# Kernel optimization log

Hardware: AMD Instinct MI355X
Metric: run time of the kernel (lower is better)

Reference implementation:

```python
import jax, jax.numpy as jnp
import numpy as np

B, P1, P2 = 16, 25, 24          # batch, patch-grid rows (+cls row), cols
E0, E1, E2 = 8, 8, 16           # 3-way factorized embed dim (total 1024)
H1, H2, H3 = 2, 2, 4            # 3-way head split (16 heads)
X, Y, Z = E0 // H1, E1 // H2, E2 // H3   # per-head factor dims (4,4,4)
SCALE = float((X * Y * Z) ** -0.5)        # head_dim = 64


def _tcl(x, w0, w1, w2, b):
    # Tensor Contraction Layer: mode-wise linear maps on the 3 embed modes.
    return jnp.einsum('bpqxyz,ax,cy,dz->bpqacd', x, w0, w1, w2) + b


def setup_inputs() -> dict:
    key = jax.random.key(0)
    ks = jax.random.split(key, 17)
    inp = {"x": jax.random.normal(ks[0], (B, P1, P2, E0, E1, E2), jnp.float32)}
    i = 1
    for nm in ("q", "k", "v", "o"):
        inp[f"{nm}_w0"] = jax.random.normal(ks[i], (E0, E0), jnp.float32) * (E0 ** -0.5); i += 1
        inp[f"{nm}_w1"] = jax.random.normal(ks[i], (E1, E1), jnp.float32) * (E1 ** -0.5); i += 1
        inp[f"{nm}_w2"] = jax.random.normal(ks[i], (E2, E2), jnp.float32) * (E2 ** -0.5); i += 1
        inp[f"{nm}_b"] = jax.random.normal(ks[i], (E0, E1, E2), jnp.float32) * 0.02; i += 1
    return inp


def _split_heads(t):
    t = t.reshape(B, P1, P2, X, H1, Y, H2, Z, H3)
    return t.transpose(0, 1, 2, 4, 6, 8, 3, 5, 7)


def reference(x,
              q_w0, q_w1, q_w2, q_b,
              k_w0, k_w1, k_w2, k_b,
              v_w0, v_w1, v_w2, v_b,
              o_w0, o_w1, o_w2, o_b):
    q = _tcl(x, q_w0, q_w1, q_w2, q_b)
    k = _tcl(x, k_w0, k_w1, k_w2, k_b)
    v = _tcl(x, v_w0, v_w1, v_w2, v_b)
    Q, K, V = _split_heads(q), _split_heads(k), _split_heads(v)
    # scores over all (p1,p2) x (m,n) token pairs, per (h1,h2,h3) head
    attn = jnp.einsum('bpqdefxyz,bmndefxyz->bdefpqmn', Q, K) * SCALE
    a = attn.reshape(B, H1, H2, H3, P1, P2, P1 * P2)
    a = jax.nn.softmax(a, axis=-1).reshape(attn.shape)
    out = jnp.einsum('bdefpqmn,bmndefxyz->bdefpqxyz', a, V)
    # b h1 h2 h3 p q x y z -> b p q (x h1)(y h2)(z h3)
    out = out.transpose(0, 4, 5, 6, 1, 7, 2, 8, 3).reshape(B, P1, P2, E0, E1, E2)
    return _tcl(out, o_w0, o_w1, o_w2, o_b)
```

## Files before the change

kernel.cpp:

```cpp
#include <hip/hip_runtime.h>

#define S   600
#define NB  16
#define NH  16
#define HD  64
#define QSCALE 0.18033688011112042f

#define LDT 20

typedef _Float16 f16x8 __attribute__((ext_vector_type(8)));
typedef float f32x4 __attribute__((ext_vector_type(4)));

__global__ __launch_bounds__(256) void tcl_qkv_kernel(
    const float* __restrict__ x,
    const float* __restrict__ qw0, const float* __restrict__ qw1,
    const float* __restrict__ qw2, const float* __restrict__ qb,
    const float* __restrict__ kw0, const float* __restrict__ kw1,
    const float* __restrict__ kw2, const float* __restrict__ kb,
    const float* __restrict__ vw0, const float* __restrict__ vw1,
    const float* __restrict__ vw2, const float* __restrict__ vb,
    _Float16* __restrict__ Qh, _Float16* __restrict__ Kh,
    _Float16* __restrict__ Vh)
{
  __shared__ __align__(16) float t1s[4][64 * LDT];
  __shared__ __align__(16) float t2s[4][64 * LDT];

  const int tid = threadIdx.x;
  const int wv = tid >> 6, lane = tid & 63;
  const int tok = blockIdx.x * 4 + wv;
  const int b = tok / S, t = tok - b * S;
  const int q = lane >> 3, zp = lane & 7;
  float* __restrict__ t1 = t1s[wv];
  float* __restrict__ t2 = t2s[wv];

  float2 xc[8];
  #pragma unroll
  for (int xx = 0; xx < 8; ++xx)
    xc[xx] = *(const float2*)&x[(size_t)tok * 1024 + xx * 128 + q * 16 + zp * 2];

  const int xs = lane >> 4;
  const int h1 = (lane >> 3) & 1;
  const int cc = lane & 7;
  const int ys = cc >> 1, h2 = cc & 1;

  const float* W0[3] = {qw0, kw0, vw0};
  const float* W1[3] = {qw1, kw1, vw1};
  const float* W2[3] = {qw2, kw2, vw2};
  const float* BB[3] = {qb, kb, vb};
  _Float16* OUT[3] = {Qh, Kh, Vh};

  #pragma unroll
  for (int p = 0; p < 3; ++p) {
    const float* __restrict__ w0 = W0[p];
    const float* __restrict__ w1 = W1[p];
    const float* __restrict__ w2 = W2[p];
    const float* __restrict__ bb = BB[p];
    _Float16* __restrict__ op = OUT[p];

    #pragma unroll
    for (int a = 0; a < 8; ++a) {
      float2 r = make_float2(0.f, 0.f);
      #pragma unroll
      for (int xx = 0; xx < 8; ++xx) {
        const float w = w0[a * 8 + xx];
        r.x = fmaf(w, xc[xx].x, r.x);
        r.y = fmaf(w, xc[xx].y, r.y);
      }
      *(float2*)&t1[(a * 8 + q) * LDT + zp * 2] = r;
    }
    __builtin_amdgcn_wave_barrier();

    float2 t1r[8];
    #pragma unroll
    for (int y = 0; y < 8; ++y)
      t1r[y] = *(float2*)&t1[(q * 8 + y) * LDT + zp * 2];
    #pragma unroll
    for (int c = 0; c < 8; ++c) {
      float2 r = make_float2(0.f, 0.f);
      #pragma unroll
      for (int y = 0; y < 8; ++y) {
        const float w = w1[c * 8 + y];
        r.x = fmaf(w, t1r[y].x, r.x);
        r.y = fmaf(w, t1r[y].y, r.y);
      }
      *(float2*)&t2[(q * 8 + c) * LDT + zp * 2] = r;
    }
    __builtin_amdgcn_wave_barrier();

    float t2r[16];
    #pragma unroll
    for (int k = 0; k < 4; ++k)
      *(float4*)&t2r[k * 4] = *(float4*)&t2[lane * LDT + k * 4];
    float bias[16];
    #pragma unroll
    for (int k = 0; k < 4; ++k)
      *(float4*)&bias[k * 4] = *(const float4*)&bb[lane * 16 + k * 4];
    float o[16];
    #pragma unroll
    for (int d = 0; d < 16; ++d) {
      float acc = 0.f;
      #pragma unroll
      for (int j = 0; j < 16; ++j)
        acc = fmaf(w2[d * 16 + j], t2r[j], acc);
      o[d] = acc + bias[d];
    }
    const float sc = (p == 0) ? QSCALE : 1.0f;
    #pragma unroll
    for (int h3 = 0; h3 < 4; ++h3) {
      union { _Float16 hh[4]; uint2 u; } pk;
      #pragma unroll
      for (int z = 0; z < 4; ++z)
        pk.hh[z] = (_Float16)(o[4 * z + h3] * sc);
      const int head = h1 * 8 + h2 * 4 + h3;
      *(uint2*)&op[((size_t)((b * NH + head) * S + t)) * HD + xs * 16 + ys * 4]
          = pk.u;
    }
    __builtin_amdgcn_wave_barrier();
  }
}

__global__ __launch_bounds__(256) void vtrans_kernel(
    const _Float16* __restrict__ Vh, _Float16* __restrict__ Vt)
{
  __shared__ __align__(16) _Float16 tile[64 * 64];
  const int tid = threadIdx.x;
  const int tt = blockIdx.x, h = blockIdx.y, b = blockIdx.z;
  const size_t rbase = (size_t)(b * NH + h) * S * HD;
  const size_t wbase = (size_t)(b * NH + h) * HD * S;
  const int t0 = tt * 64;

  #pragma unroll
  for (int hp = 0; hp < 2; ++hp) {
    const int u = hp * 256 + tid;
    const int r = u >> 3, ch = u & 7;
    f16x8 v = {0, 0, 0, 0, 0, 0, 0, 0};
    if (t0 + r < S) v = *(const f16x8*)&Vh[rbase + (size_t)(t0 + r) * HD + ch * 8];
    *(f16x8*)&tile[r * 64 + ((ch ^ ((r ^ (r >> 3)) & 7)) * 8)] = v;
  }
  __syncthreads();
  #pragma unroll
  for (int hp = 0; hp < 2; ++hp) {
    const int w = hp * 256 + tid;
    const int d = w >> 3, tc = w & 7;
    if (t0 + tc * 8 + 8 <= S) {
      const int cd = d >> 3;
      union { _Float16 hh[8]; f16x8 v; } g;
      #pragma unroll
      for (int e = 0; e < 8; ++e) {
        const int r = tc * 8 + e;
        g.hh[e] = tile[r * 64 + ((cd ^ ((r ^ (r >> 3)) & 7)) * 8) + (d & 7)];
      }
      *(f16x8*)&Vt[wbase + (size_t)d * S + t0 + tc * 8] = g.v;
    }
  }
}

__device__ __forceinline__ void gload16(const _Float16* g, _Float16* l) {
  __builtin_amdgcn_global_load_lds(
      (const __attribute__((address_space(1))) unsigned int*)g,
      (__attribute__((address_space(3))) unsigned int*)l, 16, 0, 0);
}

template<bool TAIL>
__device__ __forceinline__ void attn_step(
    const _Float16* __restrict__ Ks, const _Float16* __restrict__ Vs,
    _Float16* __restrict__ Pw,
    const f16x8 qf0, const f16x8 qf1,
    f32x4 (&po)[4], float& mrow, float& lrow,
    const int lr, const int lg)
{
  constexpr int NMT = TAIL ? 2 : 4;
  f32x4 accs[NMT];
  #pragma unroll
  for (int mt = 0; mt < NMT; ++mt) accs[mt] = (f32x4){0.f, 0.f, 0.f, 0.f};
  __builtin_amdgcn_s_setprio(1);
  #pragma unroll
  for (int c = 0; c < 2; ++c) {
    const f16x8 qf = c ? qf1 : qf0;
    #pragma unroll
    for (int mt = 0; mt < NMT; ++mt) {
      const int krow = mt * 16 + lr;
      const f16x8 kf = *(const f16x8*)
          &Ks[krow * 64 + (((4 * c + lg) ^ (krow & 7)) * 8)];
      accs[mt] = __builtin_amdgcn_mfma_f32_16x16x32_f16(kf, qf, accs[mt], 0, 0, 0);
    }
  }
  __builtin_amdgcn_s_setprio(0);
  float sv[NMT][4];
  #pragma unroll
  for (int mt = 0; mt < NMT; ++mt)
    #pragma unroll
    for (int r = 0; r < 4; ++r) {
      float s = accs[mt][r];
      if (TAIL && mt == 1) s = (lg < 2) ? s : -1e30f;
      sv[mt][r] = s;
    }
  float tmax;
  {
    const float a = fmaxf(fmaxf(sv[0][0], sv[0][1]), fmaxf(sv[0][2], sv[0][3]));
    const float b = fmaxf(fmaxf(sv[1][0], sv[1][1]), fmaxf(sv[1][2], sv[1][3]));
    if (TAIL) {
      tmax = fmaxf(a, b);
    } else {
      const float c2 = fmaxf(fmaxf(sv[2][0], sv[2][1]), fmaxf(sv[2][2], sv[2][3]));
      const float d2 = fmaxf(fmaxf(sv[3][0], sv[3][1]), fmaxf(sv[3][2], sv[3][3]));
      tmax = fmaxf(fmaxf(a, b), fmaxf(c2, d2));
    }
  }
  tmax = fmaxf(tmax, __shfl_xor(tmax, 16));
  tmax = fmaxf(tmax, __shfl_xor(tmax, 32));
  if (!__all(tmax - mrow <= 11.0f)) {
    const float mn = fmaxf(mrow, tmax);
    const float corr = __builtin_amdgcn_exp2f(mrow - mn);
    lrow *= corr;
    #pragma unroll
    for (int dt = 0; dt < 4; ++dt) {
      po[dt][0] *= corr; po[dt][1] *= corr;
      po[dt][2] *= corr; po[dt][3] *= corr;
    }
    mrow = mn;
  }
  _Float16 ph[NMT][4];
  float rsv[NMT];
  #pragma unroll
  for (int mt = 0; mt < NMT; ++mt) {
    const float e0 = __builtin_amdgcn_exp2f(sv[mt][0] - mrow);
    const float e1 = __builtin_amdgcn_exp2f(sv[mt][1] - mrow);
    const float e2 = __builtin_amdgcn_exp2f(sv[mt][2] - mrow);
    const float e3 = __builtin_amdgcn_exp2f(sv[mt][3] - mrow);
    ph[mt][0] = (_Float16)e0; ph[mt][1] = (_Float16)e1;
    ph[mt][2] = (_Float16)e2; ph[mt][3] = (_Float16)e3;
    rsv[mt] = (e0 + e1) + (e2 + e3);
  }
  float rs = TAIL ? (rsv[0] + rsv[1]) : ((rsv[0] + rsv[1]) + (rsv[2] + rsv[3]));
  rs += __shfl_xor(rs, 16);
  rs += __shfl_xor(rs, 32);
  lrow += rs;
  #pragma unroll
  for (int mt = 0; mt < NMT; ++mt) {
    union { _Float16 hh[4]; unsigned long long u; } pk;
    pk.hh[0] = ph[mt][0]; pk.hh[1] = ph[mt][1];
    pk.hh[2] = ph[mt][2]; pk.hh[3] = ph[mt][3];
    const int idx = lr * 64 + (((2 * mt + (lg >> 1)) ^ (lr & 7)) * 8)
                  + (lg & 1) * 4;
    *(unsigned long long*)&Pw[idx] = pk.u;
  }
  __builtin_amdgcn_wave_barrier();
  __builtin_amdgcn_s_setprio(1);
  #pragma unroll
  for (int c = 0; c < (TAIL ? 1 : 2); ++c) {
    const f16x8 pf = *(const f16x8*)&Pw[lr * 64 + (((4 * c + lg) ^ (lr & 7)) * 8)];
    #pragma unroll
    for (int dt = 0; dt < 4; ++dt) {
      const int drow = dt * 16 + lr;
      const f16x8 vf = *(const f16x8*)
          &Vs[drow * 64 + (((4 * c + lg) ^ (drow & 7)) * 8)];
      po[dt] = __builtin_amdgcn_mfma_f32_16x16x32_f16(vf, pf, po[dt], 0, 0, 0);
    }
  }
  __builtin_amdgcn_s_setprio(0);
}

__global__ __launch_bounds__(256, 4) void attn_mfma_kernel(
    const _Float16* __restrict__ Qh, const _Float16* __restrict__ Kh,
    const _Float16* __restrict__ Vt, float* __restrict__ Og)
{
  __shared__ __align__(16) union {
    struct {
      _Float16 K[2][64 * 64];
      _Float16 V[2][64 * 64];
      _Float16 P[4][16 * 64];
    } m;
    float ot[4][64 * 17];
  } sm;

  const int tid = threadIdx.x;
  const int lane = tid & 63;
  const int wv = tid >> 6;
  const int id = blockIdx.x;
  const int idx = id >> 3;
  const int bh = (id & 7) * 32 + idx / 10;
  const int qt = idx - (idx / 10) * 10;
  const size_t base  = (size_t)bh * S * HD;
  const size_t vbase = (size_t)bh * HD * S;
  const int lr = lane & 15;
  const int lg = lane >> 4;

  const int qrow_l = qt * 64 + wv * 16 + lr;
  const int qrow = (qrow_l < S) ? qrow_l : (S - 1);
  const f16x8 qf0 = *(const f16x8*)&Qh[base + (size_t)qrow * HD + lg * 8];
  const f16x8 qf1 = *(const f16x8*)&Qh[base + (size_t)qrow * HD + 32 + lg * 8];

  f32x4 po[4] = {{0.f,0.f,0.f,0.f},{0.f,0.f,0.f,0.f},
                 {0.f,0.f,0.f,0.f},{0.f,0.f,0.f,0.f}};
  float mrow = -1e30f, lrow = 0.f;

  const int sr = lane >> 3, ss = lane & 7;
  const int swz8 = (ss ^ sr) * 8;
  const int c0 = wv, c1 = wv + 4;
  const _Float16* kg0 = Kh + base + (size_t)(c0 * 8 + sr) * HD + swz8;
  const _Float16* kg1 = Kh + base + (size_t)(c1 * 8 + sr) * HD + swz8;
  const _Float16* vg0 = Vt + vbase + (size_t)(c0 * 8 + sr) * S + swz8;
  const _Float16* vg1 = Vt + vbase + (size_t)(c1 * 8 + sr) * S + swz8;

  auto gload_tile = [&](int kt, int b) {
    const int kb = kt * 64;
    gload16(kg0 + (size_t)kb * HD, &sm.m.K[b][c0 * 512]);
    gload16(kg1 + (size_t)kb * HD, &sm.m.K[b][c1 * 512]);
    gload16(vg0 + kb, &sm.m.V[b][c0 * 512]);
    gload16(vg1 + kb, &sm.m.V[b][c1 * 512]);
  };

  gload_tile(0, 0);
  #pragma unroll 2
  for (int kt = 0; kt < 9; ++kt) {
    const int b = kt & 1;
    __syncthreads();
    gload_tile(kt + 1, b ^ 1);
    attn_step<false>(&sm.m.K[b][0], &sm.m.V[b][0], &sm.m.P[wv][0],
                     qf0, qf1, po, mrow, lrow, lr, lg);
  }
  __syncthreads();
  for (int u = tid; u < 320; u += 256) {
    const int row = u / 5, kc = 3 + u % 5;
    *(f16x8*)&sm.m.V[1][row * 64 + ((kc ^ (row & 7)) * 8)] =
        (f16x8){0, 0, 0, 0, 0, 0, 0, 0};
  }
  __syncthreads();
  attn_step<true>(&sm.m.K[1][0], &sm.m.V[1][0], &sm.m.P[wv][0],
                  qf0, qf1, po, mrow, lrow, lr, lg);
  __syncthreads();

  const float invl = 1.0f / lrow;
  #pragma unroll
  for (int dt = 0; dt < 4; ++dt)
    #pragma unroll
    for (int r = 0; r < 4; ++r)
      sm.ot[wv][(dt * 16 + 4 * lg + r) * 17 + lr] = po[dt][r] * invl;
  __builtin_amdgcn_wave_barrier();
  #pragma unroll
  for (int ps = 0; ps < 4; ++ps) {
    const int qr = ps * 4 + lg;
    const int gq = qt * 64 + wv * 16 + qr;
    if (gq < S) {
      const int d0 = lr * 4;
      float4 o4;
      o4.x = sm.ot[wv][(d0 + 0) * 17 + qr];
      o4.y = sm.ot[wv][(d0 + 1) * 17 + qr];
      o4.z = sm.ot[wv][(d0 + 2) * 17 + qr];
      o4.w = sm.ot[wv][(d0 + 3) * 17 + qr];
      *(float4*)&Og[base + (size_t)gq * HD + d0] = o4;
    }
  }
}

__global__ __launch_bounds__(256) void tcl_out_kernel(
    const float* __restrict__ Og,
    const float* __restrict__ ow0, const float* __restrict__ ow1,
    const float* __restrict__ ow2, const float* __restrict__ ob,
    float* __restrict__ out)
{
  __shared__ __align__(16) float t1s[4][64 * LDT];
  __shared__ __align__(16) float t2s[4][64 * LDT];

  const int tid = threadIdx.x;
  const int wv = tid >> 6, lane = tid & 63;
  const int tok = blockIdx.x * 4 + wv;
  const int b = tok / S, t = tok - b * S;
  const int q = lane >> 3, zp = lane & 7;
  float* __restrict__ t1 = t1s[wv];
  float* __restrict__ t2 = t2s[wv];

  float2 xc[8];
  {
    const int h2g = q & 1, yg = q >> 1;
    const int h3g = 2 * (zp & 1), zg = zp >> 1;
    #pragma unroll
    for (int xx = 0; xx < 8; ++xx) {
      const int headb = (xx & 1) * 8 + h2g * 4 + h3g;
      const size_t off = ((size_t)((b * NH + headb) * S + t)) * HD
                       + (xx >> 1) * 16 + yg * 4 + zg;
      xc[xx].x = Og[off];
      xc[xx].y = Og[off + (size_t)S * HD];
    }
  }

  #pragma unroll
  for (int a = 0; a < 8; ++a) {
    float2 r = make_float2(0.f, 0.f);
    #pragma unroll
    for (int xx = 0; xx < 8; ++xx) {
      const float w = ow0[a * 8 + xx];
      r.x = fmaf(w, xc[xx].x, r.x);
      r.y = fmaf(w, xc[xx].y, r.y);
    }
    *(float2*)&t1[(a * 8 + q) * LDT + zp * 2] = r;
  }
  __builtin_amdgcn_wave_barrier();

  float2 t1r[8];
  #pragma unroll
  for (int y = 0; y < 8; ++y)
    t1r[y] = *(float2*)&t1[(q * 8 + y) * LDT + zp * 2];
  #pragma unroll
  for (int c = 0; c < 8; ++c) {
    float2 r = make_float2(0.f, 0.f);
    #pragma unroll
    for (int y = 0; y < 8; ++y) {
      const float w = ow1[c * 8 + y];
      r.x = fmaf(w, t1r[y].x, r.x);
      r.y = fmaf(w, t1r[y].y, r.y);
    }
    *(float2*)&t2[(q * 8 + c) * LDT + zp * 2] = r;
  }
  __builtin_amdgcn_wave_barrier();

  float t2r[16];
  #pragma unroll
  for (int k = 0; k < 4; ++k)
    *(float4*)&t2r[k * 4] = *(float4*)&t2[lane * LDT + k * 4];
  float bias[16];
  #pragma unroll
  for (int k = 0; k < 4; ++k)
    *(float4*)&bias[k * 4] = *(const float4*)&ob[lane * 16 + k * 4];
  float o[16];
  #pragma unroll
  for (int d = 0; d < 16; ++d) {
    float acc = 0.f;
    #pragma unroll
    for (int j = 0; j < 16; ++j)
      acc = fmaf(ow2[d * 16 + j], t2r[j], acc);
    o[d] = acc + bias[d];
  }
  #pragma unroll
  for (int k = 0; k < 4; ++k) {
    const float4 res = make_float4(o[4 * k], o[4 * k + 1],
                                   o[4 * k + 2], o[4 * k + 3]);
    *(float4*)&out[(size_t)tok * 1024 + lane * 16 + k * 4] = res;
  }
}

extern "C" void kernel_launch(void* const* d_in, const int* in_sizes, int n_in,
                              void* d_out, int out_size, void* d_ws, size_t ws_size,
                              hipStream_t stream) {
  const float* x   = (const float*)d_in[0];
  const float* qw0 = (const float*)d_in[1];
  const float* qw1 = (const float*)d_in[2];
  const float* qw2 = (const float*)d_in[3];
  const float* qb  = (const float*)d_in[4];
  const float* kw0 = (const float*)d_in[5];
  const float* kw1 = (const float*)d_in[6];
  const float* kw2 = (const float*)d_in[7];
  const float* kb  = (const float*)d_in[8];
  const float* vw0 = (const float*)d_in[9];
  const float* vw1 = (const float*)d_in[10];
  const float* vw2 = (const float*)d_in[11];
  const float* vb  = (const float*)d_in[12];
  const float* ow0 = (const float*)d_in[13];
  const float* ow1 = (const float*)d_in[14];
  const float* ow2 = (const float*)d_in[15];
  const float* ob  = (const float*)d_in[16];

  const size_t N = (size_t)NB * NH * S * HD;
  _Float16* Qh  = (_Float16*)d_ws;
  _Float16* Kh  = Qh + N;
  _Float16* Vth = Kh + N;
  _Float16* Vh  = Vth + N;
  float*    O   = (float*)Vh;

  tcl_qkv_kernel<<<dim3(NB * S / 4), 256, 0, stream>>>(
      x, qw0, qw1, qw2, qb, kw0, kw1, kw2, kb, vw0, vw1, vw2, vb, Qh, Kh, Vh);
  vtrans_kernel<<<dim3(10, NH, NB), 256, 0, stream>>>(Vh, Vth);
  attn_mfma_kernel<<<dim3(2560), 256, 0, stream>>>(Qh, Kh, Vth, O);
  tcl_out_kernel<<<dim3(NB * S / 4), 256, 0, stream>>>(O, ow0, ow1, ow2, ob,
                                                       (float*)d_out);
}
```

Before: 119.1 us.

## Switch attention to 32x32x16 MFMA with 32 query rows per wave

Rewrites the attention inner step to use 32x32x16 f16 MFMA instead of 16x16x32, giving each wave 32 query rows and each block 128, which halves the grid to 1280 blocks. Each K/V tile read from LDS now serves twice as many query rows, and the per-row softmax shuffles drop to a single xor. The P buffer, output staging layout and tail masking are reworked to match. In exchange, per-thread register use rises (two 16-float score accumulators plus two 16-float outputs), which may reduce occupancy, and the coarser 128-row tiling wastes more work on the final 600-row tile.

```diff
diff --git a/kernel.cpp b/kernel.cpp
--- a/kernel.cpp
+++ b/kernel.cpp
@@ -10,6 +10,7 @@
 
 typedef _Float16 f16x8 __attribute__((ext_vector_type(8)));
 typedef float f32x4 __attribute__((ext_vector_type(4)));
+typedef float f32x16 __attribute__((ext_vector_type(16)));
 
 __global__ __launch_bounds__(256) void tcl_qkv_kernel(
     const float* __restrict__ x,
@@ -161,104 +162,116 @@
       (__attribute__((address_space(3))) unsigned int*)l, 16, 0, 0);
 }
 
+#define ZERO16 {0.f,0.f,0.f,0.f,0.f,0.f,0.f,0.f,0.f,0.f,0.f,0.f,0.f,0.f,0.f,0.f}
+
 template<bool TAIL>
-__device__ __forceinline__ void attn_step(
+__device__ __forceinline__ void attn_step32(
     const _Float16* __restrict__ Ks, const _Float16* __restrict__ Vs,
     _Float16* __restrict__ Pw,
-    const f16x8 qf0, const f16x8 qf1,
-    f32x4 (&po)[4], float& mrow, float& lrow,
-    const int lr, const int lg)
+    const f16x8 (&qf)[4],
+    f32x16 (&po)[2], float& mrow, float& lrow,
+    const int lq, const int lh)
 {
-  constexpr int NMT = TAIL ? 2 : 4;
-  f32x4 accs[NMT];
-  #pragma unroll
-  for (int mt = 0; mt < NMT; ++mt) accs[mt] = (f32x4){0.f, 0.f, 0.f, 0.f};
+  const int ksw = lq & 7;
+  f32x16 a0 = ZERO16, a1 = ZERO16;
   __builtin_amdgcn_s_setprio(1);
   #pragma unroll
-  for (int c = 0; c < 2; ++c) {
-    const f16x8 qf = c ? qf1 : qf0;
-    #pragma unroll
-    for (int mt = 0; mt < NMT; ++mt) {
-      const int krow = mt * 16 + lr;
-      const f16x8 kf = *(const f16x8*)
-          &Ks[krow * 64 + (((4 * c + lg) ^ (krow & 7)) * 8)];
-      accs[mt] = __builtin_amdgcn_mfma_f32_16x16x32_f16(kf, qf, accs[mt], 0, 0, 0);
+  for (int kc = 0; kc < 4; ++kc) {
+    const int slot = ((kc * 2 + lh) ^ ksw) * 8;
+    const f16x8 k0 = *(const f16x8*)&Ks[lq * 64 + slot];
+    a0 = __builtin_amdgcn_mfma_f32_32x32x16_f16(k0, qf[kc], a0, 0, 0, 0);
+    if (!TAIL) {
+      const f16x8 k1 = *(const f16x8*)&Ks[(32 + lq) * 64 + slot];
+      a1 = __builtin_amdgcn_mfma_f32_32x32x16_f16(k1, qf[kc], a1, 0, 0, 0);
     }
   }
   __builtin_amdgcn_s_setprio(0);
-  float sv[NMT][4];
-  #pragma unroll
-  for (int mt = 0; mt < NMT; ++mt)
-    #pragma unroll
-    for (int r = 0; r < 4; ++r) {
-      float s = accs[mt][r];
-      if (TAIL && mt == 1) s = (lg < 2) ? s : -1e30f;
-      sv[mt][r] = s;
-    }
-  float tmax;
-  {
-    const float a = fmaxf(fmaxf(sv[0][0], sv[0][1]), fmaxf(sv[0][2], sv[0][3]));
-    const float b = fmaxf(fmaxf(sv[1][0], sv[1][1]), fmaxf(sv[1][2], sv[1][3]));
-    if (TAIL) {
-      tmax = fmaxf(a, b);
-    } else {
-      const float c2 = fmaxf(fmaxf(sv[2][0], sv[2][1]), fmaxf(sv[2][2], sv[2][3]));
-      const float d2 = fmaxf(fmaxf(sv[3][0], sv[3][1]), fmaxf(sv[3][2], sv[3][3]));
-      tmax = fmaxf(fmaxf(a, b), fmaxf(c2, d2));
-    }
-  }
-  tmax = fmaxf(tmax, __shfl_xor(tmax, 16));
+  float sv0[16], sv1[16];
+  float tmax = -1e30f;
+  #pragma unroll
+  for (int r = 0; r < 16; ++r) {
+    float s = a0[r];
+    if (TAIL && r >= 12) s = -1e30f;
+    sv0[r] = s;
+    tmax = fmaxf(tmax, s);
+  }
+  if (!TAIL) {
+    #pragma unroll
+    for (int r = 0; r < 16; ++r) { sv1[r] = a1[r]; tmax = fmaxf(tmax, sv1[r]); }
+  }
   tmax = fmaxf(tmax, __shfl_xor(tmax, 32));
   if (!__all(tmax - mrow <= 11.0f)) {
     const float mn = fmaxf(mrow, tmax);
     const float corr = __builtin_amdgcn_exp2f(mrow - mn);
     lrow *= corr;
-    #pragma unroll
-    for (int dt = 0; dt < 4; ++dt) {
-      po[dt][0] *= corr; po[dt][1] *= corr;
-      po[dt][2] *= corr; po[dt][3] *= corr;
-    }
+    po[0] *= corr;
+    po[1] *= corr;
     mrow = mn;
   }
-  _Float16 ph[NMT][4];
-  float rsv[NMT];
-  #pragma unroll
-  for (int mt = 0; mt < NMT; ++mt) {
-    const float e0 = __builtin_amdgcn_exp2f(sv[mt][0] - mrow);
-    const float e1 = __builtin_amdgcn_exp2f(sv[mt][1] - mrow);
-    const float e2 = __builtin_amdgcn_exp2f(sv[mt][2] - mrow);
-    const float e3 = __builtin_amdgcn_exp2f(sv[mt][3] - mrow);
-    ph[mt][0] = (_Float16)e0; ph[mt][1] = (_Float16)e1;
-    ph[mt][2] = (_Float16)e2; ph[mt][3] = (_Float16)e3;
-    rsv[mt] = (e0 + e1) + (e2 + e3);
-  }
-  float rs = TAIL ? (rsv[0] + rsv[1]) : ((rsv[0] + rsv[1]) + (rsv[2] + rsv[3]));
-  rs += __shfl_xor(rs, 16);
+  float rs = 0.f;
+  {
+    _Float16 ph[16];
+    #pragma unroll
+    for (int r = 0; r < 16; ++r) {
+      const float e = __builtin_amdgcn_exp2f(sv0[r] - mrow);
+      rs += e;
+      ph[r] = (_Float16)e;
+    }
+    #pragma unroll
+    for (int g = 0; g < 4; ++g) {
+      union { _Float16 hh[4]; unsigned long long u; } pk;
+      pk.hh[0] = ph[4*g]; pk.hh[1] = ph[4*g+1];
+      pk.hh[2] = ph[4*g+2]; pk.hh[3] = ph[4*g+3];
+      *(unsigned long long*)&Pw[lq * 32 + ((g ^ (lq & 3)) * 8) + lh * 4] = pk.u;
+    }
+    __builtin_amdgcn_wave_barrier();
+    __builtin_amdgcn_s_setprio(1);
+    #pragma unroll
+    for (int kc2 = 0; kc2 < 2; ++kc2) {
+      const f16x8 pf = *(const f16x8*)
+          &Pw[lq * 32 + (((kc2 * 2 + lh) ^ (lq & 3)) * 8)];
+      #pragma unroll
+      for (int db = 0; db < 2; ++db) {
+        const f16x8 vf = *(const f16x8*)
+            &Vs[(db * 32 + lq) * 64 + (((kc2 * 2 + lh) ^ ksw) * 8)];
+        po[db] = __builtin_amdgcn_mfma_f32_32x32x16_f16(vf, pf, po[db], 0, 0, 0);
+      }
+    }
+    __builtin_amdgcn_s_setprio(0);
+  }
+  if (!TAIL) {
+    __builtin_amdgcn_wave_barrier();
+    _Float16 ph[16];
+    #pragma unroll
+    for (int r = 0; r < 16; ++r) {
+      const float e = __builtin_amdgcn_exp2f(sv1[r] - mrow);
+      rs += e;
+      ph[r] = (_Float16)e;
+    }
+    #pragma unroll
+    for (int g = 0; g < 4; ++g) {
+      union { _Float16 hh[4]; unsigned long long u; } pk;
+      pk.hh[0] = ph[4*g]; pk.hh[1] = ph[4*g+1];
+      pk.hh[2] = ph[4*g+2]; pk.hh[3] = ph[4*g+3];
+      *(unsigned long long*)&Pw[lq * 32 + ((g ^ (lq & 3)) * 8) + lh * 4] = pk.u;
+    }
+    __builtin_amdgcn_wave_barrier();
+    __builtin_amdgcn_s_setprio(1);
+    #pragma unroll
+    for (int kc2 = 0; kc2 < 2; ++kc2) {
+      const f16x8 pf = *(const f16x8*)
+          &Pw[lq * 32 + (((kc2 * 2 + lh) ^ (lq & 3)) * 8)];
+      #pragma unroll
+      for (int db = 0; db < 2; ++db) {
+        const f16x8 vf = *(const f16x8*)
+            &Vs[(db * 32 + lq) * 64 + (((4 + kc2 * 2 + lh) ^ ksw) * 8)];
+        po[db] = __builtin_amdgcn_mfma_f32_32x32x16_f16(vf, pf, po[db], 0, 0, 0);
+      }
+    }
+    __builtin_amdgcn_s_setprio(0);
+  }
   rs += __shfl_xor(rs, 32);
   lrow += rs;
-  #pragma unroll
-  for (int mt = 0; mt < NMT; ++mt) {
-    union { _Float16 hh[4]; unsigned long long u; } pk;
-    pk.hh[0] = ph[mt][0]; pk.hh[1] = ph[mt][1];
-    pk.hh[2] = ph[mt][2]; pk.hh[3] = ph[mt][3];
-    const int idx = lr * 64 + (((2 * mt + (lg >> 1)) ^ (lr & 7)) * 8)
-                  + (lg & 1) * 4;
-    *(unsigned long long*)&Pw[idx] = pk.u;
-  }
-  __builtin_amdgcn_wave_barrier();
-  __builtin_amdgcn_s_setprio(1);
-  #pragma unroll
-  for (int c = 0; c < (TAIL ? 1 : 2); ++c) {
-    const f16x8 pf = *(const f16x8*)&Pw[lr * 64 + (((4 * c + lg) ^ (lr & 7)) * 8)];
-    #pragma unroll
-    for (int dt = 0; dt < 4; ++dt) {
-      const int drow = dt * 16 + lr;
-      const f16x8 vf = *(const f16x8*)
-          &Vs[drow * 64 + (((4 * c + lg) ^ (drow & 7)) * 8)];
-      po[dt] = __builtin_amdgcn_mfma_f32_16x16x32_f16(vf, pf, po[dt], 0, 0, 0);
-    }
-  }
-  __builtin_amdgcn_s_setprio(0);
 }
 
 __global__ __launch_bounds__(256, 4) void attn_mfma_kernel(
@@ -269,9 +282,9 @@
     struct {
       _Float16 K[2][64 * 64];
       _Float16 V[2][64 * 64];
-      _Float16 P[4][16 * 64];
+      _Float16 P[4][32 * 32];
     } m;
-    float ot[4][64 * 17];
+    float ot[4][32 * 68];
   } sm;
 
   const int tid = threadIdx.x;
@@ -279,20 +292,21 @@
   const int wv = tid >> 6;
   const int id = blockIdx.x;
   const int idx = id >> 3;
-  const int bh = (id & 7) * 32 + idx / 10;
-  const int qt = idx - (idx / 10) * 10;
+  const int bh = (id & 7) * 32 + idx / 5;
+  const int qt = idx - (idx / 5) * 5;
   const size_t base  = (size_t)bh * S * HD;
   const size_t vbase = (size_t)bh * HD * S;
-  const int lr = lane & 15;
-  const int lg = lane >> 4;
-
-  const int qrow_l = qt * 64 + wv * 16 + lr;
+  const int lq = lane & 31;
+  const int lh = lane >> 5;
+
+  const int qrow_l = qt * 128 + wv * 32 + lq;
   const int qrow = (qrow_l < S) ? qrow_l : (S - 1);
-  const f16x8 qf0 = *(const f16x8*)&Qh[base + (size_t)qrow * HD + lg * 8];
-  const f16x8 qf1 = *(const f16x8*)&Qh[base + (size_t)qrow * HD + 32 + lg * 8];
-
-  f32x4 po[4] = {{0.f,0.f,0.f,0.f},{0.f,0.f,0.f,0.f},
-                 {0.f,0.f,0.f,0.f},{0.f,0.f,0.f,0.f}};
+  f16x8 qf[4];
+  #pragma unroll
+  for (int kc = 0; kc < 4; ++kc)
+    qf[kc] = *(const f16x8*)&Qh[base + (size_t)qrow * HD + kc * 16 + lh * 8];
+
+  f32x16 po[2] = {ZERO16, ZERO16};
   float mrow = -1e30f, lrow = 0.f;
 
   const int sr = lane >> 3, ss = lane & 7;
@@ -317,39 +331,43 @@
     const int b = kt & 1;
     __syncthreads();
     gload_tile(kt + 1, b ^ 1);
-    attn_step<false>(&sm.m.K[b][0], &sm.m.V[b][0], &sm.m.P[wv][0],
-                     qf0, qf1, po, mrow, lrow, lr, lg);
+    attn_step32<false>(&sm.m.K[b][0], &sm.m.V[b][0], &sm.m.P[wv][0],
+                       qf, po, mrow, lrow, lq, lh);
   }
   __syncthreads();
   for (int u = tid; u < 320; u += 256) {
-    const int row = u / 5, kc = 3 + u % 5;
-    *(f16x8*)&sm.m.V[1][row * 64 + ((kc ^ (row & 7)) * 8)] =
+    const int row = u / 5, ch = 3 + u % 5;
+    *(f16x8*)&sm.m.V[1][row * 64 + ((ch ^ (row & 7)) * 8)] =
         (f16x8){0, 0, 0, 0, 0, 0, 0, 0};
   }
   __syncthreads();
-  attn_step<true>(&sm.m.K[1][0], &sm.m.V[1][0], &sm.m.P[wv][0],
-                  qf0, qf1, po, mrow, lrow, lr, lg);
+  attn_step32<true>(&sm.m.K[1][0], &sm.m.V[1][0], &sm.m.P[wv][0],
+                    qf, po, mrow, lrow, lq, lh);
   __syncthreads();
 
   const float invl = 1.0f / lrow;
-  #pragma unroll
-  for (int dt = 0; dt < 4; ++dt)
-    #pragma unroll
-    for (int r = 0; r < 4; ++r)
-      sm.ot[wv][(dt * 16 + 4 * lg + r) * 17 + lr] = po[dt][r] * invl;
+  float* otw = &sm.ot[wv][0];
+  #pragma unroll
+  for (int db = 0; db < 2; ++db)
+    #pragma unroll
+    for (int g = 0; g < 4; ++g) {
+      float4 v;
+      v.x = po[db][4*g]   * invl;
+      v.y = po[db][4*g+1] * invl;
+      v.z = po[db][4*g+2] * invl;
+      v.w = po[db][4*g+3] * invl;
+      *(float4*)&otw[lq * 68 + db * 32 + g * 8 + lh * 4] = v;
+    }
   __builtin_amdgcn_wave_barrier();
-  #pragma unroll
-  for (int ps = 0; ps < 4; ++ps) {
-    const int qr = ps * 4 + lg;
-    const int gq = qt * 64 + wv * 16 + qr;
+  {
+    const int r = lane >> 1, half = lane & 1;
+    const int gq = qt * 128 + wv * 32 + r;
     if (gq < S) {
-      const int d0 = lr * 4;
-      float4 o4;
-      o4.x = sm.ot[wv][(d0 + 0) * 17 + qr];
-      o4.y = sm.ot[wv][(d0 + 1) * 17 + qr];
-      o4.z = sm.ot[wv][(d0 + 2) * 17 + qr];
-      o4.w = sm.ot[wv][(d0 + 3) * 17 + qr];
-      *(float4*)&Og[base + (size_t)gq * HD + d0] = o4;
+      #pragma unroll
+      for (int k2 = 0; k2 < 8; ++k2) {
+        const float4 v = *(float4*)&otw[r * 68 + half * 32 + k2 * 4];
+        *(float4*)&Og[base + (size_t)gq * HD + half * 32 + k2 * 4] = v;
+      }
     }
   }
 }
@@ -471,7 +489,7 @@
   tcl_qkv_kernel<<<dim3(NB * S / 4), 256, 0, stream>>>(
       x, qw0, qw1, qw2, qb, kw0, kw1, kw2, kb, vw0, vw1, vw2, vb, Qh, Kh, Vh);
   vtrans_kernel<<<dim3(10, NH, NB), 256, 0, stream>>>(Vh, Vth);
-  attn_mfma_kernel<<<dim3(2560), 256, 0, stream>>>(Qh, Kh, Vth, O);
+  attn_mfma_kernel<<<dim3(1280), 256, 0, stream>>>(Qh, Kh, Vth, O);
   tcl_out_kernel<<<dim3(NB * S / 4), 256, 0, stream>>>(O, ow0, ow1, ow2, ob,
                                                        (float*)d_out);
 }
```

Result: no change. 119.2 us (+0.1%).
